# Performance work log

Measured on AMD Instinct MI355X. Metric: run time of the kernel, lower is better.

Reference implementation:

```python
import jax, jax.numpy as jnp
import numpy as np

N, E, IN_DIM, EMBED_DIM, HID_DIM = 10000, 320000, 128, 128, 64
NEG_SLOPE = 0.2


def setup_inputs() -> dict:
    key = jax.random.key(0)
    ks = jax.random.split(key, 7)
    x = jax.random.normal(ks[0], (N, IN_DIM), dtype=jnp.float32)
    edge_index = jax.random.randint(ks[1], (2, E), 0, N, dtype=jnp.int64)
    dense_w = jax.random.normal(ks[2], (IN_DIM, EMBED_DIM), dtype=jnp.float32) / np.sqrt(IN_DIM)
    dense_b = jnp.zeros((EMBED_DIM,), dtype=jnp.float32)
    gat_w = jax.random.normal(ks[3], (EMBED_DIM, HID_DIM), dtype=jnp.float32) / np.sqrt(EMBED_DIM)
    att_src = jax.random.normal(ks[4], (HID_DIM,), dtype=jnp.float32) * 0.1
    att_dst = jax.random.normal(ks[5], (HID_DIM,), dtype=jnp.float32) * 0.1
    gat_b = jnp.zeros((HID_DIM,), dtype=jnp.float32)
    return {"x": x, "edge_index": edge_index, "dense_w": dense_w, "dense_b": dense_b,
            "gat_w": gat_w, "att_src": att_src, "att_dst": att_dst, "gat_b": gat_b}


def reference(x, edge_index, dense_w, dense_b, gat_w, att_src, att_dst, gat_b):
    n = x.shape[0]
    # dense + relu
    h = jax.nn.relu(x @ dense_w + dense_b)            # [N, embed]
    # GATConv (heads=1): linear transform
    z = h @ gat_w                                     # [N, hid]
    # add self loops (PyG default)
    loops = jnp.arange(n, dtype=edge_index.dtype)
    src = jnp.concatenate([edge_index[0], loops])     # [E+N] message source j
    dst = jnp.concatenate([edge_index[1], loops])     # [E+N] message target i
    a_src = z @ att_src                               # [N]
    a_dst = z @ att_dst                               # [N]
    e = jax.nn.leaky_relu(a_src[src] + a_dst[dst], NEG_SLOPE)  # [E+N]
    # segment softmax over incoming edges of each target node
    m = jax.ops.segment_max(e, dst, num_segments=n)
    ex = jnp.exp(e - m[dst])
    denom = jax.ops.segment_sum(ex, dst, num_segments=n)
    alpha = ex / denom[dst]                           # [E+N]
    embed_x = jax.ops.segment_sum(alpha[:, None] * z[src], dst, num_segments=n) + gat_b  # [N, hid]
    # pairwise sigmoid similarity
    sim = jax.nn.sigmoid(embed_x @ embed_x.T)         # [N, N]
    return sim, embed_x
```

## Files before the change

kernel.cpp:

```cpp
#include <hip/hip_runtime.h>
#include <math.h>

#define N_NODES 10000
#define E_EDGES 320000
#define IN_DIM 128
#define EMB 128
#define HID 64
#define NEG_SLOPE 0.2f

typedef __attribute__((ext_vector_type(8))) short short8;
typedef __attribute__((ext_vector_type(4))) short short4_t;
typedef __attribute__((ext_vector_type(4))) float floatx4;
typedef __attribute__((ext_vector_type(4))) int   intx4;
typedef __attribute__((ext_vector_type(2))) int   intx2;

__device__ __forceinline__ short f2bf(float f) {
    unsigned u = __float_as_uint(f);
    unsigned r = u + 0x7fffu + ((u >> 16) & 1u);
    return (short)(r >> 16);
}

__device__ __forceinline__ float sigmoidf_fast(float v) {
    return __builtin_amdgcn_rcpf(1.f + __expf(-v));
}

__global__ __launch_bounds__(256) void dense_gat_kernel(
    const float* __restrict__ x, const float* __restrict__ dw,
    const float* __restrict__ db, const float* __restrict__ gw,
    const float* __restrict__ asv, const float* __restrict__ adv,
    float* __restrict__ z, float* __restrict__ a_src, float* __restrict__ a_dst)
{
    __shared__ float xs[16][IN_DIM];
    __shared__ float hs[16][EMB];
    __shared__ float wsm[32 * 128];
    const int t = threadIdx.x;
    const int row0 = blockIdx.x * 16;

    #pragma unroll
    for (int r = 0; r < 2; ++r) {
        const int idx = t + r * 256;
        const int row = idx >> 5, c4 = idx & 31;
        *(floatx4*)&xs[row][c4 * 4] =
            *(const floatx4*)&x[(row0 + row) * IN_DIM + c4 * 4];
    }

    const int col = t & 127, rb = (t >> 7) * 8;
    float acc[8];
    {
        const float bias = db[col];
        #pragma unroll
        for (int r = 0; r < 8; ++r) acc[r] = bias;
    }
    for (int ch = 0; ch < 4; ++ch) {
        __syncthreads();
        #pragma unroll
        for (int r = 0; r < 4; ++r) {
            const int idx = t + r * 256;
            const int row = idx >> 5, c4 = idx & 31;
            *(floatx4*)&wsm[row * 128 + c4 * 4] =
                *(const floatx4*)&dw[(ch * 32 + row) * EMB + c4 * 4];
        }
        __syncthreads();
        #pragma unroll
        for (int jg = 0; jg < 8; ++jg) {
            const int jb = jg * 4;
            floatx4 xr[8];
            #pragma unroll
            for (int r = 0; r < 8; ++r)
                xr[r] = *(const floatx4*)&xs[rb + r][ch * 32 + jb];
            float wv[4];
            #pragma unroll
            for (int k = 0; k < 4; ++k) wv[k] = wsm[(jb + k) * 128 + col];
            #pragma unroll
            for (int k = 0; k < 4; ++k)
                #pragma unroll
                for (int r = 0; r < 8; ++r) acc[r] = fmaf(xr[r][k], wv[k], acc[r]);
        }
    }
    #pragma unroll
    for (int r = 0; r < 8; ++r) hs[rb + r][col] = fmaxf(acc[r], 0.f);

    const int col2 = t & 63, rb2 = (t >> 6) * 4;
    float acc2[4] = {0.f, 0.f, 0.f, 0.f};
    for (int ch = 0; ch < 2; ++ch) {
        __syncthreads();
        #pragma unroll
        for (int r = 0; r < 4; ++r) {
            const int idx = t + r * 256;
            const int row = idx >> 4, c4 = idx & 15;
            *(floatx4*)&wsm[row * 64 + c4 * 4] =
                *(const floatx4*)&gw[(ch * 64 + row) * HID + c4 * 4];
        }
        __syncthreads();
        #pragma unroll
        for (int kg = 0; kg < 16; ++kg) {
            const int kb = kg * 4;
            floatx4 hr[4];
            #pragma unroll
            for (int r = 0; r < 4; ++r)
                hr[r] = *(const floatx4*)&hs[rb2 + r][ch * 64 + kb];
            float gv[4];
            #pragma unroll
            for (int k = 0; k < 4; ++k) gv[k] = wsm[(kb + k) * 64 + col2];
            #pragma unroll
            for (int k = 0; k < 4; ++k)
                #pragma unroll
                for (int r = 0; r < 4; ++r) acc2[r] = fmaf(hr[r][k], gv[k], acc2[r]);
        }
    }

    const float as_c = asv[col2], ad_c = adv[col2];
    #pragma unroll
    for (int r = 0; r < 4; ++r) {
        z[(row0 + rb2 + r) * HID + col2] = acc2[r];
        float ps = acc2[r] * as_c;
        float pd = acc2[r] * ad_c;
        #pragma unroll
        for (int off = 32; off > 0; off >>= 1) {
            ps += __shfl_down(ps, off, 64);
            pd += __shfl_down(pd, off, 64);
        }
        if ((t & 63) == 0) {
            a_src[row0 + rb2 + r] = ps;
            a_dst[row0 + rb2 + r] = pd;
        }
    }
}

__global__ __launch_bounds__(256) void count_kernel(
    const int* __restrict__ ei, int* __restrict__ cnt)
{
    const int e = blockIdx.x * blockDim.x + threadIdx.x;
    const int total = E_EDGES + N_NODES;
    if (e >= total) return;
    int s, d;
    if (e < E_EDGES) { s = ei[e]; d = ei[E_EDGES + e]; }
    else             { s = d = e - E_EDGES; }
    if ((unsigned)s >= N_NODES || (unsigned)d >= N_NODES) return;
    atomicAdd(&cnt[d], 1);
}

__global__ __launch_bounds__(256) void scan_kernel(
    const int* __restrict__ cnt, int* __restrict__ offs, int* __restrict__ cursor)
{
    __shared__ int scnt[10240];
    __shared__ int part[256];
    const int t = threadIdx.x;
    #pragma unroll
    for (int r = 0; r < 10; ++r) {
        const int i4 = t + r * 256;
        intx4 v = {0, 0, 0, 0};
        if (i4 < 2500) v = *(const intx4*)&cnt[i4 * 4];
        *(intx4*)&scnt[i4 * 4] = v;
    }
    __syncthreads();
    const int base = t * 40;
    int vals[40];
    int local = 0;
    #pragma unroll
    for (int i = 0; i < 40; ++i) { vals[i] = scnt[base + i]; local += vals[i]; }
    part[t] = local;
    __syncthreads();
    for (int off = 1; off < 256; off <<= 1) {
        const int v = (t >= off) ? part[t - off] : 0;
        __syncthreads();
        part[t] += v;
        __syncthreads();
    }
    int running = (t == 0) ? 0 : part[t - 1];
    #pragma unroll
    for (int i = 0; i < 40; ++i) {
        const int idx = base + i;
        if (idx < N_NODES) { offs[idx] = running; cursor[idx] = running; }
        running += vals[i];
    }
    if (t == 255) offs[N_NODES] = running;
}

__global__ __launch_bounds__(256) void scatter_kernel(
    const int* __restrict__ ei, const float* __restrict__ a_src,
    const float* __restrict__ a_dst, int* __restrict__ cursor,
    intx2* __restrict__ se)
{
    const int e = blockIdx.x * blockDim.x + threadIdx.x;
    const int total = E_EDGES + N_NODES;
    if (e >= total) return;
    int s, d;
    if (e < E_EDGES) { s = ei[e]; d = ei[E_EDGES + e]; }
    else             { s = d = e - E_EDGES; }
    if ((unsigned)s >= N_NODES || (unsigned)d >= N_NODES) return;
    float v = a_src[s] + a_dst[d];
    v = (v > 0.f) ? v : NEG_SLOPE * v;
    const float w = __expf(v);
    const int pos = atomicAdd(&cursor[d], 1);
    intx2 p;
    p[0] = s;
    p[1] = __float_as_int(w);
    se[pos] = p;
}

__global__ __launch_bounds__(256) void aggregate_kernel(
    const int* __restrict__ offs, const intx2* __restrict__ se,
    const float* __restrict__ z, const float* __restrict__ gb,
    float* __restrict__ emb)
{
    const int wid  = (blockIdx.x * blockDim.x + threadIdx.x) >> 6;
    const int lane = threadIdx.x & 63;
    if (wid >= N_NODES) return;
    const int g  = lane >> 4;
    const int c4 = (lane & 15) * 4;
    const int beg = offs[wid], end = offs[wid + 1];
    floatx4 acc = {0.f, 0.f, 0.f, 0.f};
    float sw = 0.f;
    for (int i = beg + g; i < end; i += 4) {
        const intx2 p = se[i];
        const floatx4 zv = *(const floatx4*)&z[p[0] * HID + c4];
        const float w = __int_as_float(p[1]);
        acc += zv * w;
        sw  += w;
    }
    #pragma unroll
    for (int off = 16; off <= 32; off <<= 1) {
        #pragma unroll
        for (int k = 0; k < 4; ++k) acc[k] += __shfl_xor(acc[k], off, 64);
        sw += __shfl_xor(sw, off, 64);
    }
    if (g == 0) {
        const floatx4 gv = *(const floatx4*)&gb[c4];
        floatx4 r;
        #pragma unroll
        for (int k = 0; k < 4; ++k) r[k] = acc[k] / sw + gv[k];
        *(floatx4*)&emb[wid * HID + c4] = r;
    }
}

#define SROW 72
#define SCR_STRIDE 133
__global__ __launch_bounds__(256) void sim_kernel(
    const float* __restrict__ emb, float* __restrict__ sim)
{
    __shared__ float smem[128 * SCR_STRIDE];
    short* const As = (short*)smem;
    short* const Bs = (short*)smem + 128 * SROW;
    const int t    = threadIdx.x;
    const int lane = t & 63;
    const int wave = t >> 6;
    const int wm   = (wave >> 1) * 64;
    const int wn   = (wave & 1) * 64;
    const int l15  = lane & 15;
    const int quad = lane >> 4;

    int bi, bj;
    {
        const int gx = blockIdx.x, gy = blockIdx.y;
        if (gy <= gx) { bi = gy; bj = gx; }
        else          { bi = 40 + gx; bj = 79 + gx - gy; }
    }

    #pragma unroll
    for (int round = 0; round < 8; ++round) {
        const int idx = t + round * 256;
        const int row = idx >> 4, c4 = idx & 15;
        int gr = bi * 128 + row; if (gr > N_NODES - 1) gr = N_NODES - 1;
        int gc = bj * 128 + row; if (gc > N_NODES - 1) gc = N_NODES - 1;
        const floatx4 a = *(const floatx4*)&emb[gr * HID + c4 * 4];
        const floatx4 b = *(const floatx4*)&emb[gc * HID + c4 * 4];
        short4_t sa, sb;
        #pragma unroll
        for (int j = 0; j < 4; ++j) { sa[j] = f2bf(a[j]); sb[j] = f2bf(b[j]); }
        *(short4_t*)&As[row * SROW + c4 * 4] = sa;
        *(short4_t*)&Bs[row * SROW + c4 * 4] = sb;
    }
    __syncthreads();

    short8 afrag[4][2];
    #pragma unroll
    for (int ti = 0; ti < 4; ++ti)
        #pragma unroll
        for (int ks = 0; ks < 2; ++ks)
            afrag[ti][ks] = *(const short8*)&As[(wm + ti * 16 + l15) * SROW +
                                                ks * 32 + quad * 8];

    floatx4 acc[4][4];
    const floatx4 zero = {0.f, 0.f, 0.f, 0.f};
    #pragma unroll
    for (int ti = 0; ti < 4; ++ti)
        #pragma unroll
        for (int tj = 0; tj < 4; ++tj) acc[ti][tj] = zero;

    #pragma unroll
    for (int tj = 0; tj < 4; ++tj) {
        const short8 bf0 = *(const short8*)&Bs[(wn + tj * 16 + l15) * SROW + quad * 8];
        const short8 bf1 = *(const short8*)&Bs[(wn + tj * 16 + l15) * SROW + 32 + quad * 8];
        #pragma unroll
        for (int ti = 0; ti < 4; ++ti) {
            acc[ti][tj] = __builtin_amdgcn_mfma_f32_16x16x32_bf16(
                afrag[ti][0], bf0, acc[ti][tj], 0, 0, 0);
            acc[ti][tj] = __builtin_amdgcn_mfma_f32_16x16x32_bf16(
                afrag[ti][1], bf1, acc[ti][tj], 0, 0, 0);
        }
    }
    __syncthreads();

    #pragma unroll
    for (int ti = 0; ti < 4; ++ti)
        #pragma unroll
        for (int reg = 0; reg < 4; ++reg)
            #pragma unroll
            for (int tj = 0; tj < 4; ++tj)
                smem[(wm + ti * 16 + quad * 4 + reg) * SCR_STRIDE +
                     wn + tj * 16 + l15] = sigmoidf_fast(acc[ti][tj][reg]);
    __syncthreads();

    #pragma unroll
    for (int round = 0; round < 16; ++round) {
        const int idx = t + round * 256;
        const int rr = idx >> 5, cq = idx & 31;
        const int grow = bi * 128 + rr;
        const int gcol = bj * 128 + cq * 4;
        if (grow < N_NODES && gcol < N_NODES) {
            const floatx4 v4 = *(const floatx4*)&smem[rr * SCR_STRIDE + cq * 4];
            *(floatx4*)&sim[(unsigned)grow * N_NODES + gcol] = v4;
        }
    }
    if (bi != bj) {
        #pragma unroll
        for (int round = 0; round < 16; ++round) {
            const int idx = t + round * 256;
            const int rr = idx >> 5, cq = idx & 31;
            const int trow = bj * 128 + rr;
            const int tcol = bi * 128 + cq * 4;
            if (trow < N_NODES && tcol < N_NODES) {
                floatx4 v4;
                #pragma unroll
                for (int m = 0; m < 4; ++m)
                    v4[m] = smem[(cq * 4 + m) * SCR_STRIDE + rr];
                *(floatx4*)&sim[(unsigned)trow * N_NODES + tcol] = v4;
            }
        }
    }
}

extern "C" void kernel_launch(void* const* d_in, const int* in_sizes, int n_in,
                              void* d_out, int out_size, void* d_ws, size_t ws_size,
                              hipStream_t stream)
{
    const float* x   = (const float*)d_in[0];
    const int*   ei  = (const int*)d_in[1];
    const float* dw  = (const float*)d_in[2];
    const float* db  = (const float*)d_in[3];
    const float* gw  = (const float*)d_in[4];
    const float* asv = (const float*)d_in[5];
    const float* adv = (const float*)d_in[6];
    const float* gb  = (const float*)d_in[7];

    float* out = (float*)d_out;
    float* sim = out;
    float* emb = out + (size_t)N_NODES * N_NODES;

    const size_t need = 1350002u * sizeof(float);
    float* ws = (ws_size >= need) ? (float*)d_ws : out;
    float* z      = ws;
    float* a_src  = ws + 640000;
    float* a_dst  = ws + 650000;
    int*   cnt    = (int*)(ws + 660000);
    int*   offs   = (int*)(ws + 670000);
    int*   cursor = (int*)(ws + 680001);
    intx2* se     = (intx2*)(ws + 690002);

    hipMemsetAsync(cnt, 0, N_NODES * sizeof(int), stream);

    dense_gat_kernel<<<N_NODES / 16, 256, 0, stream>>>(x, dw, db, gw, asv, adv,
                                                       z, a_src, a_dst);

    const int total_edges = E_EDGES + N_NODES;
    const int eb = (total_edges + 255) / 256;
    count_kernel<<<eb, 256, 0, stream>>>(ei, cnt);
    scan_kernel<<<1, 256, 0, stream>>>(cnt, offs, cursor);
    scatter_kernel<<<eb, 256, 0, stream>>>(ei, a_src, a_dst, cursor, se);
    aggregate_kernel<<<(N_NODES * 64 + 255) / 256, 256, 0, stream>>>(
        offs, se, z, gb, emb);

    dim3 grid(79, 40);
    sim_kernel<<<grid, 256, 0, stream>>>(emb, sim);
}
```

Baseline: 563.9 us.

## Fuse dense and count kernels, widen scan, drop symmetric sim tiling

Merges the edge-count pass into the dense/GAT kernel using extra blocks, and rewrites the scan to use 1024 threads reading global memory directly. The sim kernel no longer exploits symmetry. It launches the full 79x79 grid, and each wave computes a 32x128 strip with less shared memory. Stores use nontemporal hints and occupancy is raised via launch bounds. This removes the strided transposed-write path and a launch, at the cost of doubling the MFMA work in the similarity matmul.

```diff
diff --git a/kernel.cpp b/kernel.cpp
--- a/kernel.cpp
+++ b/kernel.cpp
@@ -8,10 +8,13 @@
 #define HID 64
 #define NEG_SLOPE 0.2f
 
+#define DG_BLOCKS 625
+#define CNT_BLOCKS 665
+#define TOTAL_EDGES (E_EDGES + N_NODES)
+
 typedef __attribute__((ext_vector_type(8))) short short8;
 typedef __attribute__((ext_vector_type(4))) short short4_t;
 typedef __attribute__((ext_vector_type(4))) float floatx4;
-typedef __attribute__((ext_vector_type(4))) int   intx4;
 typedef __attribute__((ext_vector_type(2))) int   intx2;
 
 __device__ __forceinline__ short f2bf(float f) {
@@ -24,23 +27,40 @@
     return __builtin_amdgcn_rcpf(1.f + __expf(-v));
 }
 
-__global__ __launch_bounds__(256) void dense_gat_kernel(
+__global__ __launch_bounds__(256) void dense_gat_count_kernel(
     const float* __restrict__ x, const float* __restrict__ dw,
     const float* __restrict__ db, const float* __restrict__ gw,
     const float* __restrict__ asv, const float* __restrict__ adv,
-    float* __restrict__ z, float* __restrict__ a_src, float* __restrict__ a_dst)
-{
-    __shared__ float xs[16][IN_DIM];
-    __shared__ float hs[16][EMB];
-    __shared__ float wsm[32 * 128];
+    const int* __restrict__ ei,
+    float* __restrict__ z, float* __restrict__ a_src, float* __restrict__ a_dst,
+    int* __restrict__ cnt)
+{
+    __shared__ float smem[8192];
     const int t = threadIdx.x;
-    const int row0 = blockIdx.x * 16;
+    const int b = blockIdx.x;
+
+    if (b >= DG_BLOCKS) {
+        const int nth = CNT_BLOCKS * 256;
+        for (int e = (b - DG_BLOCKS) * 256 + t; e < TOTAL_EDGES; e += nth) {
+            int s, d;
+            if (e < E_EDGES) { s = ei[e]; d = ei[E_EDGES + e]; }
+            else             { s = d = e - E_EDGES; }
+            if ((unsigned)s >= N_NODES || (unsigned)d >= N_NODES) continue;
+            atomicAdd(&cnt[d], 1);
+        }
+        return;
+    }
+
+    float* const xs  = smem;
+    float* const hs  = smem + 2048;
+    float* const wsm = smem + 4096;
+    const int row0 = b * 16;
 
     #pragma unroll
     for (int r = 0; r < 2; ++r) {
         const int idx = t + r * 256;
         const int row = idx >> 5, c4 = idx & 31;
-        *(floatx4*)&xs[row][c4 * 4] =
+        *(floatx4*)&xs[row * 128 + c4 * 4] =
             *(const floatx4*)&x[(row0 + row) * IN_DIM + c4 * 4];
     }
 
@@ -67,7 +87,7 @@
             floatx4 xr[8];
             #pragma unroll
             for (int r = 0; r < 8; ++r)
-                xr[r] = *(const floatx4*)&xs[rb + r][ch * 32 + jb];
+                xr[r] = *(const floatx4*)&xs[(rb + r) * 128 + ch * 32 + jb];
             float wv[4];
             #pragma unroll
             for (int k = 0; k < 4; ++k) wv[k] = wsm[(jb + k) * 128 + col];
@@ -78,7 +98,7 @@
         }
     }
     #pragma unroll
-    for (int r = 0; r < 8; ++r) hs[rb + r][col] = fmaxf(acc[r], 0.f);
+    for (int r = 0; r < 8; ++r) hs[(rb + r) * 128 + col] = fmaxf(acc[r], 0.f);
 
     const int col2 = t & 63, rb2 = (t >> 6) * 4;
     float acc2[4] = {0.f, 0.f, 0.f, 0.f};
@@ -98,7 +118,7 @@
             floatx4 hr[4];
             #pragma unroll
             for (int r = 0; r < 4; ++r)
-                hr[r] = *(const floatx4*)&hs[rb2 + r][ch * 64 + kb];
+                hr[r] = *(const floatx4*)&hs[(rb2 + r) * 128 + ch * 64 + kb];
             float gv[4];
             #pragma unroll
             for (int k = 0; k < 4; ++k) gv[k] = wsm[(kb + k) * 64 + col2];
@@ -127,41 +147,24 @@
     }
 }
 
-__global__ __launch_bounds__(256) void count_kernel(
-    const int* __restrict__ ei, int* __restrict__ cnt)
-{
-    const int e = blockIdx.x * blockDim.x + threadIdx.x;
-    const int total = E_EDGES + N_NODES;
-    if (e >= total) return;
-    int s, d;
-    if (e < E_EDGES) { s = ei[e]; d = ei[E_EDGES + e]; }
-    else             { s = d = e - E_EDGES; }
-    if ((unsigned)s >= N_NODES || (unsigned)d >= N_NODES) return;
-    atomicAdd(&cnt[d], 1);
-}
-
-__global__ __launch_bounds__(256) void scan_kernel(
+__global__ __launch_bounds__(1024) void scan_kernel(
     const int* __restrict__ cnt, int* __restrict__ offs, int* __restrict__ cursor)
 {
-    __shared__ int scnt[10240];
-    __shared__ int part[256];
+    __shared__ int part[1024];
     const int t = threadIdx.x;
-    #pragma unroll
-    for (int r = 0; r < 10; ++r) {
-        const int i4 = t + r * 256;
-        intx4 v = {0, 0, 0, 0};
-        if (i4 < 2500) v = *(const intx4*)&cnt[i4 * 4];
-        *(intx4*)&scnt[i4 * 4] = v;
-    }
-    __syncthreads();
-    const int base = t * 40;
-    int vals[40];
+    const int base = t * 10;
+    int vals[10];
     int local = 0;
     #pragma unroll
-    for (int i = 0; i < 40; ++i) { vals[i] = scnt[base + i]; local += vals[i]; }
+    for (int i = 0; i < 10; ++i) {
+        const int idx = base + i;
+        const int c = (idx < N_NODES) ? cnt[idx] : 0;
+        vals[i] = c;
+        local += c;
+    }
     part[t] = local;
     __syncthreads();
-    for (int off = 1; off < 256; off <<= 1) {
+    for (int off = 1; off < 1024; off <<= 1) {
         const int v = (t >= off) ? part[t - off] : 0;
         __syncthreads();
         part[t] += v;
@@ -169,12 +172,12 @@
     }
     int running = (t == 0) ? 0 : part[t - 1];
     #pragma unroll
-    for (int i = 0; i < 40; ++i) {
+    for (int i = 0; i < 10; ++i) {
         const int idx = base + i;
         if (idx < N_NODES) { offs[idx] = running; cursor[idx] = running; }
         running += vals[i];
     }
-    if (t == 255) offs[N_NODES] = running;
+    if (t == 1023) offs[N_NODES] = running;
 }
 
 __global__ __launch_bounds__(256) void scatter_kernel(
@@ -183,8 +186,7 @@
     intx2* __restrict__ se)
 {
     const int e = blockIdx.x * blockDim.x + threadIdx.x;
-    const int total = E_EDGES + N_NODES;
-    if (e >= total) return;
+    if (e >= TOTAL_EDGES) return;
     int s, d;
     if (e < E_EDGES) { s = ei[e]; d = ei[E_EDGES + e]; }
     else             { s = d = e - E_EDGES; }
@@ -235,27 +237,22 @@
 }
 
 #define SROW 72
-#define SCR_STRIDE 133
-__global__ __launch_bounds__(256) void sim_kernel(
+#define SCR 133
+__global__ __launch_bounds__(256, 4) void sim_kernel(
     const float* __restrict__ emb, float* __restrict__ sim)
 {
-    __shared__ float smem[128 * SCR_STRIDE];
+    __shared__ float smem[9216];
     short* const As = (short*)smem;
     short* const Bs = (short*)smem + 128 * SROW;
+    float* const scr = smem;
     const int t    = threadIdx.x;
     const int lane = t & 63;
     const int wave = t >> 6;
-    const int wm   = (wave >> 1) * 64;
-    const int wn   = (wave & 1) * 64;
     const int l15  = lane & 15;
     const int quad = lane >> 4;
 
-    int bi, bj;
-    {
-        const int gx = blockIdx.x, gy = blockIdx.y;
-        if (gy <= gx) { bi = gy; bj = gx; }
-        else          { bi = 40 + gx; bj = 79 + gx - gy; }
-    }
+    const int bi = blockIdx.y;
+    const int bj = blockIdx.x;
 
     #pragma unroll
     for (int round = 0; round < 8; ++round) {
@@ -273,27 +270,27 @@
     }
     __syncthreads();
 
-    short8 afrag[4][2];
-    #pragma unroll
-    for (int ti = 0; ti < 4; ++ti)
+    short8 afrag[2][2];
+    #pragma unroll
+    for (int ti = 0; ti < 2; ++ti)
         #pragma unroll
         for (int ks = 0; ks < 2; ++ks)
-            afrag[ti][ks] = *(const short8*)&As[(wm + ti * 16 + l15) * SROW +
+            afrag[ti][ks] = *(const short8*)&As[((ti * 4 + wave) * 16 + l15) * SROW +
                                                 ks * 32 + quad * 8];
 
-    floatx4 acc[4][4];
+    floatx4 acc[2][8];
     const floatx4 zero = {0.f, 0.f, 0.f, 0.f};
     #pragma unroll
-    for (int ti = 0; ti < 4; ++ti)
-        #pragma unroll
-        for (int tj = 0; tj < 4; ++tj) acc[ti][tj] = zero;
-
-    #pragma unroll
-    for (int tj = 0; tj < 4; ++tj) {
-        const short8 bf0 = *(const short8*)&Bs[(wn + tj * 16 + l15) * SROW + quad * 8];
-        const short8 bf1 = *(const short8*)&Bs[(wn + tj * 16 + l15) * SROW + 32 + quad * 8];
-        #pragma unroll
-        for (int ti = 0; ti < 4; ++ti) {
+    for (int ti = 0; ti < 2; ++ti)
+        #pragma unroll
+        for (int tj = 0; tj < 8; ++tj) acc[ti][tj] = zero;
+
+    #pragma unroll
+    for (int tj = 0; tj < 8; ++tj) {
+        const short8 bf0 = *(const short8*)&Bs[(tj * 16 + l15) * SROW + quad * 8];
+        const short8 bf1 = *(const short8*)&Bs[(tj * 16 + l15) * SROW + 32 + quad * 8];
+        #pragma unroll
+        for (int ti = 0; ti < 2; ++ti) {
             acc[ti][tj] = __builtin_amdgcn_mfma_f32_16x16x32_bf16(
                 afrag[ti][0], bf0, acc[ti][tj], 0, 0, 0);
             acc[ti][tj] = __builtin_amdgcn_mfma_f32_16x16x32_bf16(
@@ -303,41 +300,28 @@
     __syncthreads();
 
     #pragma unroll
-    for (int ti = 0; ti < 4; ++ti)
+    for (int h = 0; h < 2; ++h) {
         #pragma unroll
         for (int reg = 0; reg < 4; ++reg)
             #pragma unroll
-            for (int tj = 0; tj < 4; ++tj)
-                smem[(wm + ti * 16 + quad * 4 + reg) * SCR_STRIDE +
-                     wn + tj * 16 + l15] = sigmoidf_fast(acc[ti][tj][reg]);
-    __syncthreads();
-
-    #pragma unroll
-    for (int round = 0; round < 16; ++round) {
-        const int idx = t + round * 256;
-        const int rr = idx >> 5, cq = idx & 31;
-        const int grow = bi * 128 + rr;
-        const int gcol = bj * 128 + cq * 4;
-        if (grow < N_NODES && gcol < N_NODES) {
-            const floatx4 v4 = *(const floatx4*)&smem[rr * SCR_STRIDE + cq * 4];
-            *(floatx4*)&sim[(unsigned)grow * N_NODES + gcol] = v4;
-        }
-    }
-    if (bi != bj) {
-        #pragma unroll
-        for (int round = 0; round < 16; ++round) {
+            for (int tj = 0; tj < 8; ++tj)
+                scr[(wave * 16 + quad * 4 + reg) * SCR + tj * 16 + l15] =
+                    sigmoidf_fast(acc[h][tj][reg]);
+        __syncthreads();
+
+        #pragma unroll
+        for (int round = 0; round < 8; ++round) {
             const int idx = t + round * 256;
             const int rr = idx >> 5, cq = idx & 31;
-            const int trow = bj * 128 + rr;
-            const int tcol = bi * 128 + cq * 4;
-            if (trow < N_NODES && tcol < N_NODES) {
-                floatx4 v4;
-                #pragma unroll
-                for (int m = 0; m < 4; ++m)
-                    v4[m] = smem[(cq * 4 + m) * SCR_STRIDE + rr];
-                *(floatx4*)&sim[(unsigned)trow * N_NODES + tcol] = v4;
+            const int grow = bi * 128 + (h * 4 + (rr >> 4)) * 16 + (rr & 15);
+            const int gcol = bj * 128 + cq * 4;
+            if (grow < N_NODES && gcol < N_NODES) {
+                const floatx4 v4 = *(const floatx4*)&scr[rr * SCR + cq * 4];
+                __builtin_nontemporal_store(
+                    v4, (floatx4*)&sim[(unsigned)grow * N_NODES + gcol]);
             }
         }
+        __syncthreads();
     }
 }
 
@@ -370,17 +354,16 @@
 
     hipMemsetAsync(cnt, 0, N_NODES * sizeof(int), stream);
 
-    dense_gat_kernel<<<N_NODES / 16, 256, 0, stream>>>(x, dw, db, gw, asv, adv,
-                                                       z, a_src, a_dst);
-
-    const int total_edges = E_EDGES + N_NODES;
-    const int eb = (total_edges + 255) / 256;
-    count_kernel<<<eb, 256, 0, stream>>>(ei, cnt);
-    scan_kernel<<<1, 256, 0, stream>>>(cnt, offs, cursor);
+    dense_gat_count_kernel<<<DG_BLOCKS + CNT_BLOCKS, 256, 0, stream>>>(
+        x, dw, db, gw, asv, adv, ei, z, a_src, a_dst, cnt);
+
+    scan_kernel<<<1, 1024, 0, stream>>>(cnt, offs, cursor);
+
+    const int eb = (TOTAL_EDGES + 255) / 256;
     scatter_kernel<<<eb, 256, 0, stream>>>(ei, a_src, a_dst, cursor, se);
     aggregate_kernel<<<(N_NODES * 64 + 255) / 256, 256, 0, stream>>>(
         offs, se, z, gb, emb);
 
-    dim3 grid(79, 40);
+    dim3 grid(79, 79);
     sim_kernel<<<grid, 256, 0, stream>>>(emb, sim);
 }
```

Measured after the change: 501.9 us. 1.12x faster.
